# Optimization experiments

Hardware: AMD Instinct MI355X
Metric: run time of the kernel (lower is better)

The kernel has to match this reference:

```python
import jax, jax.numpy as jnp
import numpy as np

CODEBOOK_SIZE = 1024
CODEBOOK_DIM = 64
COMMITMENT_COST = 0.25


def setup_inputs() -> dict:
    key = jax.random.key(0)
    k_in, k_cb = jax.random.split(key)
    inputs = jax.random.normal(k_in, (64, 64, 64, CODEBOOK_DIM), dtype=jnp.float32)
    # nn.init.uniform_(weight, -1/K, 1/K)
    codebook = jax.random.uniform(
        k_cb, (CODEBOOK_SIZE, CODEBOOK_DIM), dtype=jnp.float32,
        minval=-1.0 / CODEBOOK_SIZE, maxval=1.0 / CODEBOOK_SIZE)
    return {"inputs": inputs, "codebook": codebook}


def reference(inputs, codebook):
    K, D = codebook.shape
    flat = inputs.reshape(-1, D)  # (N, D)
    distances = (
        jnp.sum(flat * flat, axis=-1, keepdims=True)
        - 2.0 * (flat @ codebook.T)
        + jnp.sum(codebook * codebook, axis=-1)[None, :]
    )
    idx = jnp.argmin(distances, axis=-1)  # (N,)
    codes = jnp.take(codebook, idx, axis=0).reshape(inputs.shape)
    # commitment loss (quantize detached)
    commitment_loss = jnp.mean(jnp.square(jax.lax.stop_gradient(codes) - inputs))
    loss = COMMITMENT_COST * commitment_loss
    # straight-through estimator
    quantize = inputs + jax.lax.stop_gradient(codes - inputs)
    # perplexity via cluster counts (equivalent to one_hot.mean(0), no NxK one-hot)
    counts = jax.ops.segment_sum(
        jnp.ones(idx.shape, dtype=inputs.dtype), idx, num_segments=K)
    avg_probs = counts / jnp.asarray(idx.shape[0], dtype=inputs.dtype)
    perplexity = jnp.exp(-jnp.sum(avg_probs * jnp.log(avg_probs + 1e-10)))
    return quantize, loss, perplexity
```

## Files before the change

kernel.cpp:

```cpp
#include <hip/hip_runtime.h>

#define NVEC (64*64*64)
#define KCB 1024
#define DIM 64
#define BATCHES 16
#define GRID 256
#define NSLOT 32

typedef __attribute__((ext_vector_type(8))) short s16x8;
typedef __attribute__((ext_vector_type(4))) float f32x4;

#define MFMA16(A, B, C) __builtin_amdgcn_mfma_f32_16x16x32_bf16((A), (B), (C), 0, 0, 0)


__global__ __launch_bounds__(256) void vq_prep(const float* __restrict__ cb,
                                               unsigned short* __restrict__ cbA,
                                               float* __restrict__ cnf,
                                               unsigned int* __restrict__ slots) {
    int q = blockIdx.x * 256 + threadIdx.x;
    ((int4*)slots)[q] = int4{0, 0, 0, 0};
    int t = q >> 7;
    int h = (q >> 6) & 1;
    int l = q & 63;
    int m = t * 16 + (l & 15);
    int d0 = h * 32 + ((l >> 4) & 3) * 8;
    const float* row = cb + (size_t)m * DIM + d0;
    unsigned short* dst = cbA + (size_t)q * 8;
    #pragma unroll
    for (int j = 0; j < 8; ++j) {
        float f = -2.0f * row[j];
        unsigned u = __float_as_uint(f);
        dst[j] = (unsigned short)((u + 0x7fffu + ((u >> 16) & 1u)) >> 16);
    }
    if (q < KCB) {
        const float* r2 = cb + (size_t)q * DIM;
        double s = 0.0;
        for (int d = 0; d < DIM; ++d) { double c = (double)r2[d]; s = fma(c, c, s); }
        cnf[q] = (float)s;
    }
}

__global__ __launch_bounds__(1024) void vq_main(const float* __restrict__ inp,
                                                const unsigned short* __restrict__ cbA,
                                                const float* __restrict__ cnf,
                                                const float* __restrict__ cb,
                                                float* __restrict__ out,
                                                float* __restrict__ partials,
                                                unsigned int* __restrict__ slots) {
    __shared__ unsigned short xf[2][512][8];
    __shared__ float xnp[2][512];
    __shared__ float sred[64][17];
    __shared__ unsigned int histS[KCB];
    __shared__ float lossL[64];

    const int tid  = threadIdx.x;
    const int lane = tid & 63;
    const int wv   = tid >> 6;
    const int l15  = lane & 15;
    const int g    = lane >> 4;
    const int gi   = g * 4;
    const int blockbase = blockIdx.x * (BATCHES * 64);

    const int cvt_vt    = tid >> 7;
    const int cvt_h     = (tid >> 6) & 1;
    const int cvt_l     = tid & 63;
    const int cvt_vec   = cvt_vt * 16 + (cvt_l & 15);
    const int cvt_d0    = cvt_h * 32 + (cvt_l >> 4) * 8;
    const int cvt_slice = cvt_h * 4 + (cvt_l >> 4);

    histS[tid] = 0u;

    float4 x0{}, x1{};
    if (tid < 512) {
        const float* xp = inp + (size_t)(blockbase + cvt_vec) * DIM + cvt_d0;
        x0 = ((const float4*)xp)[0];
        x1 = ((const float4*)xp)[1];
    }

    const s16x8* __restrict__ Ap = (const s16x8*)cbA;
    s16x8 A[4][2];
    f32x4 cn[4];
    #pragma unroll
    for (int tt = 0; tt < 4; ++tt) {
        int T = wv * 4 + tt;
        A[tt][0] = Ap[(T * 2 + 0) * 64 + lane];
        A[tt][1] = Ap[(T * 2 + 1) * 64 + lane];
        cn[tt]   = *(const f32x4*)(cnf + T * 16 + gi);
    }

    float loss_acc = 0.0f;

    for (int b = 0; b < BATCHES; ++b) {
        const int buf = b & 1;
        const int vecbase = blockbase + b * 64;

        if (tid < 512) {
            float f[8] = {x0.x, x0.y, x0.z, x0.w, x1.x, x1.y, x1.z, x1.w};
            float xn = 0.f;
            unsigned wq[4];
            #pragma unroll
            for (int p = 0; p < 4; ++p) {
                xn = fmaf(f[2*p], f[2*p], xn);
                xn = fmaf(f[2*p+1], f[2*p+1], xn);
                unsigned r;
                asm("v_cvt_pk_bf16_f32 %0, %1, %2" : "=v"(r) : "v"(f[2*p]), "v"(f[2*p+1]));
                wq[p] = r;
            }
            *(int4*)&xf[buf][tid][0] = *(const int4*)wq;
            xnp[buf][cvt_vec * 8 + cvt_slice] = xn;
        }
        __syncthreads();

        if (tid < 512 && b + 1 < BATCHES) {
            const float* xp = inp + (size_t)(vecbase + 64 + cvt_vec) * DIM + cvt_d0;
            x0 = ((const float4*)xp)[0];
            x1 = ((const float4*)xp)[1];
        }

        float bestv[4];
        #pragma unroll
        for (int vt = 0; vt < 4; ++vt) {
            s16x8 xb0 = *(const s16x8*)&xf[buf][(vt * 2 + 0) * 64 + lane][0];
            s16x8 xb1 = *(const s16x8*)&xf[buf][(vt * 2 + 1) * 64 + lane][0];
            f32x4 a0 = cn[0], a1 = cn[1], a2 = cn[2], a3 = cn[3];
            a0 = MFMA16(A[0][0], xb0, a0);
            a1 = MFMA16(A[1][0], xb0, a1);
            a2 = MFMA16(A[2][0], xb0, a2);
            a3 = MFMA16(A[3][0], xb0, a3);
            a0 = MFMA16(A[0][1], xb1, a0);
            a1 = MFMA16(A[1][1], xb1, a1);
            a2 = MFMA16(A[2][1], xb1, a2);
            a3 = MFMA16(A[3][1], xb1, a3);

            float bv = 3.4e38f;
            #define PACKMIN(ACC, TT) {                                                        \
                unsigned cbase = (unsigned)(wv * 64 + (TT) * 16 + gi);                        \
                float p0 = __uint_as_float((__float_as_uint(ACC[0]) & 0xFFFFFC00u) | cbase);  \
                float p1 = __uint_as_float((__float_as_uint(ACC[1]) & 0xFFFFFC00u) | (cbase+1));\
                float p2 = __uint_as_float((__float_as_uint(ACC[2]) & 0xFFFFFC00u) | (cbase+2));\
                float p3 = __uint_as_float((__float_as_uint(ACC[3]) & 0xFFFFFC00u) | (cbase+3));\
                bv = fminf(bv, fminf(fminf(p0, p1), fminf(p2, p3))); }
            PACKMIN(a0, 0) PACKMIN(a1, 1) PACKMIN(a2, 2) PACKMIN(a3, 3)
            #undef PACKMIN
            bestv[vt] = bv;
        }

        #pragma unroll
        for (int vt = 0; vt < 4; ++vt) {
            bestv[vt] = fminf(bestv[vt], __shfl_xor(bestv[vt], 16));
            bestv[vt] = fminf(bestv[vt], __shfl_xor(bestv[vt], 32));
        }
        if (g == 0) {
            #pragma unroll
            for (int vt = 0; vt < 4; ++vt) sred[vt * 16 + l15][wv] = bestv[vt];
        }
        __syncthreads();

        {
            const int vec = tid >> 4, sl = tid & 15;
            float pb = sred[vec][sl];
            pb = fminf(pb, __shfl_xor(pb, 1));
            pb = fminf(pb, __shfl_xor(pb, 2));
            pb = fminf(pb, __shfl_xor(pb, 4));
            pb = fminf(pb, __shfl_xor(pb, 8));
            int bk = (int)(__float_as_uint(pb) & 1023u);
            float4 q = ((const float4*)cb)[bk * 16 + sl];
            ((float4*)out)[(size_t)(vecbase + vec) * 16 + sl] = q;
            if (sl == 0) {
                float xn = 0.f;
                #pragma unroll
                for (int j = 0; j < 8; ++j) xn += xnp[buf][vec * 8 + j];
                loss_acc += pb + xn;
                atomicAdd(&histS[bk], 1u);
            }
        }
    }

    if ((tid & 15) == 0) lossL[tid >> 4] = loss_acc;
    __syncthreads();
    if (tid < 64) {
        float v = lossL[tid];
        #pragma unroll
        for (int off = 32; off > 0; off >>= 1) v += __shfl_xor(v, off);
        if (tid == 0) partials[blockIdx.x] = v;
    }
    unsigned hv = histS[tid];
    if (hv) atomicAdd(&slots[(blockIdx.x & (NSLOT - 1)) * KCB + tid], hv);
}

__global__ __launch_bounds__(1024) void vq_finalize(float* __restrict__ out,
                                                    const float* __restrict__ partials,
                                                    const unsigned int* __restrict__ slots) {
    __shared__ double red[1024];
    const int tid = threadIdx.x;
    unsigned tot = 0;
    #pragma unroll
    for (int s = 0; s < NSLOT; ++s) tot += slots[s * KCB + tid];
    double p = (double)tot / (double)NVEC;
    double h = p * log(p + 1e-10);
    double ls = (tid < GRID) ? (double)partials[tid] : 0.0;

    red[tid] = ls;
    __syncthreads();
    for (int t = 512; t > 0; t >>= 1) {
        if (tid < t) red[tid] += red[tid + t];
        __syncthreads();
    }
    double loss_tot = red[0];
    __syncthreads();
    red[tid] = h;
    __syncthreads();
    for (int t = 512; t > 0; t >>= 1) {
        if (tid < t) red[tid] += red[tid + t];
        __syncthreads();
    }
    if (tid == 0) {
        out[(size_t)NVEC * DIM]     = (float)(0.25 * loss_tot / (double)((size_t)NVEC * DIM));
        out[(size_t)NVEC * DIM + 1] = (float)exp(-red[0]);
    }
}

extern "C" void kernel_launch(void* const* d_in, const int* in_sizes, int n_in,
                              void* d_out, int out_size, void* d_ws, size_t ws_size,
                              hipStream_t stream) {
    const float* inp = (const float*)d_in[0];
    const float* cb  = (const float*)d_in[1];
    float* out = (float*)d_out;

    char* ws = (char*)d_ws;
    float*          cnf      = (float*)(ws + 0);
    unsigned short* cbA      = (unsigned short*)(ws + 4096);
    float*          partials = (float*)(ws + 135168);
    unsigned int*   slots    = (unsigned int*)(ws + 136192);

    vq_prep<<<dim3(32), dim3(256), 0, stream>>>(cb, cbA, cnf, slots);
    vq_main<<<dim3(GRID), dim3(1024), 0, stream>>>(inp, cbA, cnf, cb, out,
                                                   partials, slots);
    vq_finalize<<<dim3(1), dim3(1024), 0, stream>>>(out, partials, slots);
}
```

Before: 62.17 us.

## Split codebook search across blocks with separate gather/histogram kernel

The fused main kernel is replaced by two kernels. The first splits the codebook into four slices across 1024 blocks of 256 threads, and each block writes per-slice packed distance/index minima to a global buffer. The second reduces across slices, gathers codebook rows to the output, builds the histogram and accumulates the loss. This is meant to raise parallelism and occupancy, since the old grid had only 256 large blocks. The cost is that every block now re-reads the full input once per slice (four times in total), plus an extra launch and a global round trip for the intermediate minima. It also uses v_min3 for the min reduction.

```diff
diff --git a/kernel.cpp b/kernel.cpp
--- a/kernel.cpp
+++ b/kernel.cpp
@@ -3,8 +3,12 @@
 #define NVEC (64*64*64)
 #define KCB 1024
 #define DIM 64
-#define BATCHES 16
-#define GRID 256
+#define NSLICE 4
+#define VSET 1024
+#define NBATCH 16
+#define AGRID (NSLICE * (NVEC / VSET))
+#define BVEC 256
+#define BGRID (NVEC / BVEC)
 #define NSLOT 32
 
 typedef __attribute__((ext_vector_type(8))) short s16x8;
@@ -40,18 +44,13 @@
     }
 }
 
-__global__ __launch_bounds__(1024) void vq_main(const float* __restrict__ inp,
-                                                const unsigned short* __restrict__ cbA,
-                                                const float* __restrict__ cnf,
-                                                const float* __restrict__ cb,
-                                                float* __restrict__ out,
-                                                float* __restrict__ partials,
-                                                unsigned int* __restrict__ slots) {
-    __shared__ unsigned short xf[2][512][8];
-    __shared__ float xnp[2][512];
-    __shared__ float sred[64][17];
-    __shared__ unsigned int histS[KCB];
-    __shared__ float lossL[64];
+__global__ __launch_bounds__(256, 4) void vq_sliceA(const float* __restrict__ inp,
+                                                    const unsigned short* __restrict__ cbA,
+                                                    const float* __restrict__ cnf,
+                                                    unsigned int* __restrict__ pbuf,
+                                                    float* __restrict__ xnpart) {
+    __shared__ int4  xf[2][512];
+    __shared__ float sred[64][5];
 
     const int tid  = threadIdx.x;
     const int lane = tid & 63;
@@ -59,69 +58,68 @@
     const int l15  = lane & 15;
     const int g    = lane >> 4;
     const int gi   = g * 4;
-    const int blockbase = blockIdx.x * (BATCHES * 64);
-
-    const int cvt_vt    = tid >> 7;
-    const int cvt_h     = (tid >> 6) & 1;
-    const int cvt_l     = tid & 63;
-    const int cvt_vec   = cvt_vt * 16 + (cvt_l & 15);
-    const int cvt_d0    = cvt_h * 32 + (cvt_l >> 4) * 8;
-    const int cvt_slice = cvt_h * 4 + (cvt_l >> 4);
-
-    histS[tid] = 0u;
-
-    float4 x0{}, x1{};
-    if (tid < 512) {
-        const float* xp = inp + (size_t)(blockbase + cvt_vec) * DIM + cvt_d0;
-        x0 = ((const float4*)xp)[0];
-        x1 = ((const float4*)xp)[1];
-    }
+    const int slice  = blockIdx.x & 3;
+    const int vecset = blockIdx.x >> 2;
+    const size_t vsbase = (size_t)vecset * VSET;
+
+    const int cv = tid >> 2, cq = tid & 3;
+    const int c0 = ((cv >> 4) * 2 + (cq >> 1)) * 64 + ((cq & 1) * 2) * 16 + (cv & 15);
+    const int c1 = c0 + 16;
 
     const s16x8* __restrict__ Ap = (const s16x8*)cbA;
     s16x8 A[4][2];
     f32x4 cn[4];
     #pragma unroll
-    for (int tt = 0; tt < 4; ++tt) {
-        int T = wv * 4 + tt;
-        A[tt][0] = Ap[(T * 2 + 0) * 64 + lane];
-        A[tt][1] = Ap[(T * 2 + 1) * 64 + lane];
-        cn[tt]   = *(const f32x4*)(cnf + T * 16 + gi);
-    }
-
-    float loss_acc = 0.0f;
-
-    for (int b = 0; b < BATCHES; ++b) {
+    for (int t = 0; t < 4; ++t) {
+        int Tg = slice * 16 + wv * 4 + t;
+        A[t][0] = Ap[(Tg * 2 + 0) * 64 + lane];
+        A[t][1] = Ap[(Tg * 2 + 1) * 64 + lane];
+        cn[t]   = *(const f32x4*)(cnf + Tg * 16 + gi);
+    }
+
+    const float4* xp = (const float4*)(inp + (vsbase + cv) * DIM + cq * 16);
+    float4 xr0 = xp[0], xr1 = xp[1], xr2 = xp[2], xr3 = xp[3];
+    float xnacc = 0.f;
+
+    for (int b = 0; b < NBATCH; ++b) {
         const int buf = b & 1;
-        const int vecbase = blockbase + b * 64;
-
-        if (tid < 512) {
-            float f[8] = {x0.x, x0.y, x0.z, x0.w, x1.x, x1.y, x1.z, x1.w};
-            float xn = 0.f;
-            unsigned wq[4];
-            #pragma unroll
-            for (int p = 0; p < 4; ++p) {
-                xn = fmaf(f[2*p], f[2*p], xn);
-                xn = fmaf(f[2*p+1], f[2*p+1], xn);
-                unsigned r;
-                asm("v_cvt_pk_bf16_f32 %0, %1, %2" : "=v"(r) : "v"(f[2*p]), "v"(f[2*p+1]));
-                wq[p] = r;
-            }
-            *(int4*)&xf[buf][tid][0] = *(const int4*)wq;
-            xnp[buf][cvt_vec * 8 + cvt_slice] = xn;
-        }
-        __syncthreads();
-
-        if (tid < 512 && b + 1 < BATCHES) {
-            const float* xp = inp + (size_t)(vecbase + 64 + cvt_vec) * DIM + cvt_d0;
-            x0 = ((const float4*)xp)[0];
-            x1 = ((const float4*)xp)[1];
-        }
-
-        float bestv[4];
+
+        {
+            float f0 = xr0.x, f1 = xr0.y, f2 = xr0.z, f3 = xr0.w;
+            float f4 = xr1.x, f5 = xr1.y, f6 = xr1.z, f7 = xr1.w;
+            float f8 = xr2.x, f9 = xr2.y, f10 = xr2.z, f11 = xr2.w;
+            float f12 = xr3.x, f13 = xr3.y, f14 = xr3.z, f15 = xr3.w;
+            xnacc = fmaf(f0, f0, xnacc);   xnacc = fmaf(f1, f1, xnacc);
+            xnacc = fmaf(f2, f2, xnacc);   xnacc = fmaf(f3, f3, xnacc);
+            xnacc = fmaf(f4, f4, xnacc);   xnacc = fmaf(f5, f5, xnacc);
+            xnacc = fmaf(f6, f6, xnacc);   xnacc = fmaf(f7, f7, xnacc);
+            xnacc = fmaf(f8, f8, xnacc);   xnacc = fmaf(f9, f9, xnacc);
+            xnacc = fmaf(f10, f10, xnacc); xnacc = fmaf(f11, f11, xnacc);
+            xnacc = fmaf(f12, f12, xnacc); xnacc = fmaf(f13, f13, xnacc);
+            xnacc = fmaf(f14, f14, xnacc); xnacc = fmaf(f15, f15, xnacc);
+            unsigned w0, w1, w2, w3, w4, w5, w6, w7;
+            asm("v_cvt_pk_bf16_f32 %0, %1, %2" : "=v"(w0) : "v"(f0),  "v"(f1));
+            asm("v_cvt_pk_bf16_f32 %0, %1, %2" : "=v"(w1) : "v"(f2),  "v"(f3));
+            asm("v_cvt_pk_bf16_f32 %0, %1, %2" : "=v"(w2) : "v"(f4),  "v"(f5));
+            asm("v_cvt_pk_bf16_f32 %0, %1, %2" : "=v"(w3) : "v"(f6),  "v"(f7));
+            asm("v_cvt_pk_bf16_f32 %0, %1, %2" : "=v"(w4) : "v"(f8),  "v"(f9));
+            asm("v_cvt_pk_bf16_f32 %0, %1, %2" : "=v"(w5) : "v"(f10), "v"(f11));
+            asm("v_cvt_pk_bf16_f32 %0, %1, %2" : "=v"(w6) : "v"(f12), "v"(f13));
+            asm("v_cvt_pk_bf16_f32 %0, %1, %2" : "=v"(w7) : "v"(f14), "v"(f15));
+            xf[buf][c0] = int4{(int)w0, (int)w1, (int)w2, (int)w3};
+            xf[buf][c1] = int4{(int)w4, (int)w5, (int)w6, (int)w7};
+        }
+        __syncthreads();
+
+        if (b + 1 < NBATCH) {
+            const float4* np = (const float4*)(inp + (vsbase + (size_t)(b + 1) * 64 + cv) * DIM + cq * 16);
+            xr0 = np[0]; xr1 = np[1]; xr2 = np[2]; xr3 = np[3];
+        }
+
         #pragma unroll
         for (int vt = 0; vt < 4; ++vt) {
-            s16x8 xb0 = *(const s16x8*)&xf[buf][(vt * 2 + 0) * 64 + lane][0];
-            s16x8 xb1 = *(const s16x8*)&xf[buf][(vt * 2 + 1) * 64 + lane][0];
+            s16x8 xb0 = *(const s16x8*)&xf[buf][(vt * 2 + 0) * 64 + lane];
+            s16x8 xb1 = *(const s16x8*)&xf[buf][(vt * 2 + 1) * 64 + lane];
             f32x4 a0 = cn[0], a1 = cn[1], a2 = cn[2], a3 = cn[3];
             a0 = MFMA16(A[0][0], xb0, a0);
             a1 = MFMA16(A[1][0], xb0, a1);
@@ -133,63 +131,90 @@
             a3 = MFMA16(A[3][1], xb1, a3);
 
             float bv = 3.4e38f;
-            #define PACKMIN(ACC, TT) {                                                        \
-                unsigned cbase = (unsigned)(wv * 64 + (TT) * 16 + gi);                        \
-                float p0 = __uint_as_float((__float_as_uint(ACC[0]) & 0xFFFFFC00u) | cbase);  \
+            #define PACKMIN(ACC, TT) {                                                          \
+                unsigned cbase = (unsigned)((slice * 16 + wv * 4 + (TT)) * 16 + gi);            \
+                float p0 = __uint_as_float((__float_as_uint(ACC[0]) & 0xFFFFFC00u) | cbase);    \
                 float p1 = __uint_as_float((__float_as_uint(ACC[1]) & 0xFFFFFC00u) | (cbase+1));\
                 float p2 = __uint_as_float((__float_as_uint(ACC[2]) & 0xFFFFFC00u) | (cbase+2));\
                 float p3 = __uint_as_float((__float_as_uint(ACC[3]) & 0xFFFFFC00u) | (cbase+3));\
-                bv = fminf(bv, fminf(fminf(p0, p1), fminf(p2, p3))); }
+                float m01;                                                                      \
+                asm("v_min3_f32 %0, %1, %2, %3" : "=v"(m01) : "v"(p0), "v"(p1), "v"(p2));       \
+                asm("v_min3_f32 %0, %1, %2, %3" : "=v"(bv) : "v"(m01), "v"(p3), "v"(bv)); }
             PACKMIN(a0, 0) PACKMIN(a1, 1) PACKMIN(a2, 2) PACKMIN(a3, 3)
             #undef PACKMIN
-            bestv[vt] = bv;
-        }
-
-        #pragma unroll
-        for (int vt = 0; vt < 4; ++vt) {
-            bestv[vt] = fminf(bestv[vt], __shfl_xor(bestv[vt], 16));
-            bestv[vt] = fminf(bestv[vt], __shfl_xor(bestv[vt], 32));
-        }
-        if (g == 0) {
-            #pragma unroll
-            for (int vt = 0; vt < 4; ++vt) sred[vt * 16 + l15][wv] = bestv[vt];
+            bv = fminf(bv, __shfl_xor(bv, 16));
+            bv = fminf(bv, __shfl_xor(bv, 32));
+            if (g == 0) sred[vt * 16 + l15][wv] = bv;
         }
         __syncthreads();
 
         {
-            const int vec = tid >> 4, sl = tid & 15;
-            float pb = sred[vec][sl];
+            const int v = tid >> 2, slot = tid & 3;
+            float pb = sred[v][slot];
             pb = fminf(pb, __shfl_xor(pb, 1));
             pb = fminf(pb, __shfl_xor(pb, 2));
-            pb = fminf(pb, __shfl_xor(pb, 4));
-            pb = fminf(pb, __shfl_xor(pb, 8));
-            int bk = (int)(__float_as_uint(pb) & 1023u);
-            float4 q = ((const float4*)cb)[bk * 16 + sl];
-            ((float4*)out)[(size_t)(vecbase + vec) * 16 + sl] = q;
-            if (sl == 0) {
-                float xn = 0.f;
-                #pragma unroll
-                for (int j = 0; j < 8; ++j) xn += xnp[buf][vec * 8 + j];
-                loss_acc += pb + xn;
-                atomicAdd(&histS[bk], 1u);
-            }
-        }
-    }
-
-    if ((tid & 15) == 0) lossL[tid >> 4] = loss_acc;
-    __syncthreads();
-    if (tid < 64) {
-        float v = lossL[tid];
+            float pbc = __shfl(pb, (lane & 15) * 4);
+            if (lane < 16)
+                pbuf[(size_t)slice * NVEC + vsbase + (size_t)b * 64 + wv * 16 + lane] =
+                    __float_as_uint(pbc);
+        }
+    }
+
+    if (slice == 0) {
+        float v = xnacc;
         #pragma unroll
         for (int off = 32; off > 0; off >>= 1) v += __shfl_xor(v, off);
-        if (tid == 0) partials[blockIdx.x] = v;
-    }
-    unsigned hv = histS[tid];
-    if (hv) atomicAdd(&slots[(blockIdx.x & (NSLOT - 1)) * KCB + tid], hv);
+        if (lane == 0) xnpart[vecset * 4 + wv] = v;
+    }
+}
+
+__global__ __launch_bounds__(256) void vq_sliceB(const unsigned int* __restrict__ pbuf,
+                                                 const float* __restrict__ cb,
+                                                 float* __restrict__ out,
+                                                 float* __restrict__ scorepart,
+                                                 unsigned int* __restrict__ slots) {
+    __shared__ unsigned int histS[KCB];
+    __shared__ float lred[4];
+    const int tid = threadIdx.x, lane = tid & 63, wv = tid >> 6;
+    #pragma unroll
+    for (int i = 0; i < 4; ++i) histS[tid + i * 256] = 0u;
+    __syncthreads();
+
+    float sacc = 0.f;
+    const size_t vb = (size_t)blockIdx.x * BVEC;
+    const float4* cb4 = (const float4*)cb;
+    float4* out4 = (float4*)out;
+
+    for (int r = 0; r < BVEC / 16; ++r) {
+        const size_t vec = vb + r * 16 + (tid >> 4);
+        const int sl = tid & 15;
+        float pf = __uint_as_float(pbuf[(size_t)(sl & 3) * NVEC + vec]);
+        pf = fminf(pf, __shfl_xor(pf, 1));
+        pf = fminf(pf, __shfl_xor(pf, 2));
+        const int bk = (int)(__float_as_uint(pf) & 1023u);
+        float4 q = cb4[bk * 16 + sl];
+        out4[vec * 16 + sl] = q;
+        if (sl == 0) {
+            sacc += pf;
+            atomicAdd(&histS[bk], 1u);
+        }
+    }
+
+    #pragma unroll
+    for (int off = 32; off > 0; off >>= 1) sacc += __shfl_xor(sacc, off);
+    if (lane == 0) lred[wv] = sacc;
+    __syncthreads();
+    if (tid == 0) scorepart[blockIdx.x] = lred[0] + lred[1] + lred[2] + lred[3];
+    #pragma unroll
+    for (int i = 0; i < 4; ++i) {
+        unsigned hv = histS[tid + i * 256];
+        if (hv) atomicAdd(&slots[(blockIdx.x & (NSLOT - 1)) * KCB + tid + i * 256], hv);
+    }
 }
 
 __global__ __launch_bounds__(1024) void vq_finalize(float* __restrict__ out,
-                                                    const float* __restrict__ partials,
+                                                    const float* __restrict__ scorepart,
+                                                    const float* __restrict__ xnpart,
                                                     const unsigned int* __restrict__ slots) {
     __shared__ double red[1024];
     const int tid = threadIdx.x;
@@ -198,7 +223,7 @@
     for (int s = 0; s < NSLOT; ++s) tot += slots[s * KCB + tid];
     double p = (double)tot / (double)NVEC;
     double h = p * log(p + 1e-10);
-    double ls = (tid < GRID) ? (double)partials[tid] : 0.0;
+    double ls = (double)scorepart[tid] + (double)xnpart[tid];
 
     red[tid] = ls;
     __syncthreads();
@@ -228,13 +253,15 @@
     float* out = (float*)d_out;
 
     char* ws = (char*)d_ws;
-    float*          cnf      = (float*)(ws + 0);
-    unsigned short* cbA      = (unsigned short*)(ws + 4096);
-    float*          partials = (float*)(ws + 135168);
-    unsigned int*   slots    = (unsigned int*)(ws + 136192);
+    float*          cnf       = (float*)(ws + 0);
+    unsigned short* cbA       = (unsigned short*)(ws + 4096);
+    unsigned int*   pbuf      = (unsigned int*)(ws + 135168);
+    float*          xnpart    = (float*)(ws + 4329472);
+    float*          scorepart = (float*)(ws + 4333568);
+    unsigned int*   slots     = (unsigned int*)(ws + 4337664);
 
     vq_prep<<<dim3(32), dim3(256), 0, stream>>>(cb, cbA, cnf, slots);
-    vq_main<<<dim3(GRID), dim3(1024), 0, stream>>>(inp, cbA, cnf, cb, out,
-                                                   partials, slots);
-    vq_finalize<<<dim3(1), dim3(1024), 0, stream>>>(out, partials, slots);
-}
+    vq_sliceA<<<dim3(AGRID), dim3(256), 0, stream>>>(inp, cbA, cnf, pbuf, xnpart);
+    vq_sliceB<<<dim3(BGRID), dim3(256), 0, stream>>>(pbuf, cb, out, scorepart, slots);
+    vq_finalize<<<dim3(1), dim3(1024), 0, stream>>>(out, scorepart, xnpart, slots);
+}
```

Result: slower. 86.43 us (+39.0%).
